# Performance work log

Measured on AMD Instinct MI355X. Metric: run time of the kernel, lower is better.

Reference implementation:

```python
import jax, jax.numpy as jnp
import numpy as np

B, C, H, W = 8, 512, 64, 64
RED = 4
CR = C // RED  # 128

def setup_inputs() -> dict:
    key = jax.random.key(0)
    k1, k2, k3 = jax.random.split(key, 3)
    x = jax.random.normal(k1, (B, C, H, W), dtype=jnp.float32)
    # conv_in: 1x1 conv, no bias -> weight [3*CR, C]
    w_in = jax.random.normal(k2, (3 * CR, C), dtype=jnp.float32) * 0.02
    # conv_out: 1x1 conv, no bias -> weight [C, CR]
    w_out = jax.random.normal(k3, (C, CR), dtype=jnp.float32) * 0.02
    return {"x": x, "w_in": w_in, "w_out": w_out}

def reference(x, w_in, w_out):
    b, c, h, w = x.shape
    n = h * w
    xf = x.reshape(b, c, n)                         # flatten spatial -> [B,C,N]
    proj = jnp.einsum('oc,bcn->bon', w_in, xf)      # 1x1 conv_in -> [B,3*CR,N]
    emb_a, emb_b, g = jnp.split(proj, 3, axis=1)    # each [B,CR,N]
    # unscaled full self-attention over N spatial tokens
    weights = jnp.einsum('bcn,bcm->bnm', emb_a, emb_b)   # [B,N,N]
    weights = jax.nn.softmax(weights, axis=2)
    y = jnp.einsum('bnm,bcm->bnc', weights, g)           # [B,N,CR]
    y = jnp.einsum('oc,bnc->bon', w_out, y)              # 1x1 conv_out -> [B,C,N]
    return x + y.reshape(b, c, h, w)
```

## Files before the change

kernel.cpp:

```cpp
#include <hip/hip_runtime.h>


typedef __attribute__((ext_vector_type(8))) short short8;
typedef __attribute__((ext_vector_type(4))) float f32x4;
typedef __attribute__((ext_vector_type(16))) float f32x16;
typedef __attribute__((ext_vector_type(2))) unsigned int uint2v;

__device__ inline unsigned bfr(float f) {
  union { float f; unsigned u; } v; v.f = f;
  return v.u + 0x8000u;
}
__device__ inline unsigned short f2bf(float f) { return (unsigned short)(bfr(f) >> 16); }
__device__ inline unsigned pack2(float a, float b) {
  return __builtin_amdgcn_perm(bfr(b), bfr(a), 0x07060302u);
}
__device__ inline unsigned cvtpk(float a, float b) {
  unsigned r;
  asm("v_cvt_pk_bf16_f32 %0, %1, %2" : "=v"(r) : "v"(a), "v"(b));
  return r;
}
__device__ inline int sw(int row, int col, int stride_halves) {
  return row * stride_halves + ((((col >> 3) ^ (row & 7)) << 3) | (col & 7));
}
__device__ inline void load_lds16(const void* g, void* l) {
  __builtin_amdgcn_global_load_lds(
      (const __attribute__((address_space(1))) unsigned int*)g,
      (__attribute__((address_space(3))) unsigned int*)l, 16, 0, 0);
}

__global__ __launch_bounds__(256) void k_prep(const float* __restrict__ w_in,
                                              const float* __restrict__ w_out,
                                              unsigned short* __restrict__ wi,
                                              unsigned short* __restrict__ wo) {
  int i = blockIdx.x * 256 + threadIdx.x;
  const float* src;
  unsigned short* dst;
  int base;
  float s = 1.0f;
  if (i < 24576) {
    src = w_in;  dst = wi; base = i * 8;
    if (base < 128 * 512) s = 1.4426950408889634f;
  } else {
    src = w_out; dst = wo; base = (i - 24576) * 8;
  }
  float4 d0 = *(const float4*)&src[base];
  float4 d1 = *(const float4*)&src[base + 4];
  d0.x *= s; d0.y *= s; d0.z *= s; d0.w *= s;
  d1.x *= s; d1.y *= s; d1.z *= s; d1.w *= s;
  uint4 p;
  p.x = pack2(d0.x, d0.y); p.y = pack2(d0.z, d0.w);
  p.z = pack2(d1.x, d1.y); p.w = pack2(d1.z, d1.w);
  *(uint4*)&dst[base] = p;
}

__global__ __launch_bounds__(256) void k_proj(const float* __restrict__ x,
                                              const unsigned short* __restrict__ wi,
                                              unsigned short* __restrict__ ab,
                                              unsigned short* __restrict__ gC) {
  __shared__ unsigned short A_lds[128 * 64];
  __shared__ unsigned short B_lds[64 * 64];
  const int t = threadIdx.x;
  const int lane = t & 63;
  const int w = t >> 6;
  const int l15 = lane & 15;
  const int quad = lane >> 4;
  const int n0 = blockIdx.x * 64;
  const int o0 = blockIdx.y * 128;
  const int b = blockIdx.z;
  const int ch8g = t >> 5;
  const int tp = t & 31;

  f32x4 acc[2][4];
#pragma unroll
  for (int i = 0; i < 2; i++)
#pragma unroll
    for (int j = 0; j < 4; j++) acc[i][j] = (f32x4)0.f;

  for (int k0 = 0; k0 < 512; k0 += 64) {
#pragma unroll
    for (int j = 0; j < 4; j++) {
      int row = w * 32 + j * 8 + (lane >> 3);
      int gs = (lane & 7) ^ (row & 7);
      load_lds16(&wi[(size_t)(o0 + row) * 512 + k0 + gs * 8],
                 (void*)&A_lds[(w * 32 + j * 8) * 64]);
    }
    {
      float2 d[8];
#pragma unroll
      for (int j = 0; j < 8; j++)
        d[j] = *(const float2*)&x[((size_t)(b * 512 + k0 + ch8g * 8 + j)) * 4096 + n0 + tp * 2];
#pragma unroll
      for (int i = 0; i < 2; i++) {
        int r = tp * 2 + i;
        uint4 pv;
        if (i == 0) {
          pv.x = pack2(d[0].x, d[1].x); pv.y = pack2(d[2].x, d[3].x);
          pv.z = pack2(d[4].x, d[5].x); pv.w = pack2(d[6].x, d[7].x);
        } else {
          pv.x = pack2(d[0].y, d[1].y); pv.y = pack2(d[2].y, d[3].y);
          pv.z = pack2(d[4].y, d[5].y); pv.w = pack2(d[6].y, d[7].y);
        }
        *(uint4*)&B_lds[sw(r, ch8g * 8, 64)] = pv;
      }
    }
    __syncthreads();
#pragma unroll
    for (int kk = 0; kk < 64; kk += 32) {
      short8 a0 = *(const short8*)&A_lds[sw(w * 32 + l15, kk + quad * 8, 64)];
      short8 a1 = *(const short8*)&A_lds[sw(w * 32 + 16 + l15, kk + quad * 8, 64)];
#pragma unroll
      for (int ns = 0; ns < 4; ns++) {
        short8 bb = *(const short8*)&B_lds[sw(ns * 16 + l15, kk + quad * 8, 64)];
        acc[0][ns] = __builtin_amdgcn_mfma_f32_16x16x32_bf16(a0, bb, acc[0][ns], 0, 0, 0);
        acc[1][ns] = __builtin_amdgcn_mfma_f32_16x16x32_bf16(a1, bb, acc[1][ns], 0, 0, 0);
      }
    }
    __syncthreads();
  }
  if (o0 < 256) {
#pragma unroll
    for (int ms = 0; ms < 2; ms++) {
      int o = o0 + w * 32 + ms * 16 + quad * 4;
#pragma unroll
      for (int ns = 0; ns < 4; ns++) {
        int n = n0 + ns * 16 + l15;
        uint2 p;
        p.x = pack2(acc[ms][ns][0], acc[ms][ns][1]);
        p.y = pack2(acc[ms][ns][2], acc[ms][ns][3]);
        *(uint2*)&ab[((size_t)(b * 4096 + n)) * 256 + o] = p;
      }
    }
  } else {
#pragma unroll
    for (int ms = 0; ms < 2; ms++) {
      int og = w * 32 + ms * 16 + quad * 4;
#pragma unroll
      for (int ns = 0; ns < 4; ns++) {
        int n = n0 + ns * 16 + l15;
#pragma unroll
        for (int r = 0; r < 4; r++)
          gC[((size_t)(b * 128 + og + r)) * 4096 + n] = f2bf(acc[ms][ns][r]);
      }
    }
  }
}

__global__ __launch_bounds__(256, 2) void k_attn(const unsigned short* __restrict__ ab,
                                                 const unsigned short* __restrict__ gC,
                                                 unsigned short* __restrict__ yt) {
  __shared__ uint4 smem4[65536 / 16];
  unsigned short* smem_h = (unsigned short*)smem4;
  float* Obuf = (float*)smem4;
  float* lsumbuf = (float*)((char*)smem4 + 33024);
  unsigned* Pbuf = (unsigned*)((char*)smem4 + 33280);

  const int t = threadIdx.x;
  const int lane = t & 63;
  const int w = t >> 6;
  const int wr = w & 1;
  const int wc = w >> 1;
  const int l31 = lane & 31;
  const int h = lane >> 5;
  const int l7 = l31 & 7;
  const int b = blockIdx.x & 7;
  const int q0 = (blockIdx.x >> 3) * 64;

  short8 qf[8];
  {
    const unsigned short* qp = &ab[((size_t)(b * 4096 + q0 + wc * 32 + l31)) * 256 + h * 8];
#pragma unroll
    for (int ks = 0; ks < 8; ks++) qf[ks] = *(const short8*)&qp[ks * 16];
  }

  const int krow_c = w * 16 + (lane >> 4);
  const int vrow_c = w * 32 + (lane >> 3);

  auto dma_tile = [&](int kt, int buf) {
    unsigned short* Kb = smem_h + buf * 8192;
    unsigned short* Vb = smem_h + 16384 + buf * 8192;
#pragma unroll
    for (int j = 0; j < 4; j++) {
      int row = krow_c + j * 4;
      int gs = (lane & 15) ^ (row & 7);
      load_lds16(&ab[((size_t)(b * 4096 + kt + row)) * 256 + 128 + gs * 8],
                 (void*)&Kb[(w * 16 + j * 4) * 128]);
    }
#pragma unroll
    for (int j = 0; j < 4; j++) {
      int row = vrow_c + j * 8;
      int gs = (lane & 7) ^ (row & 7);
      load_lds16(&gC[((size_t)(b * 128 + row)) * 4096 + kt + gs * 8],
                 (void*)&Vb[(w * 32 + j * 8) * 64]);
    }
  };

  f32x16 O[4];
#pragma unroll
  for (int i = 0; i < 4; i++) O[i] = (f32x16)0.f;
  float ls0 = 0.f, ls1 = 0.f, ls2 = 0.f, ls3 = 0.f;
  const int rowK = wr * 32 + l31;

  dma_tile(0, 0);
  __syncthreads();

  for (int it = 0; it < 64; ++it) {
    if (it < 63) dma_tile((it + 1) * 64, (it + 1) & 1);
    const unsigned short* Kc = smem_h + (it & 1) * 8192;
    const unsigned short* Vc = smem_h + 16384 + (it & 1) * 8192;

    f32x16 accS = (f32x16)0.f;
    __builtin_amdgcn_s_setprio(1);
#pragma unroll
    for (int ks = 0; ks < 8; ks++) {
      short8 ak = *(const short8*)&Kc[rowK * 128 + (((ks * 2 + h) ^ l7) << 3)];
      accS = __builtin_amdgcn_mfma_f32_32x32x16_bf16(ak, qf[ks], accS, 0, 0, 0);
    }
    __builtin_amdgcn_s_setprio(0);

    float ps[16];
#pragma unroll
    for (int r = 0; r < 16; r++) ps[r] = __builtin_amdgcn_exp2f(accS[r]);
    ls0 += ps[0] + ps[4];  ls1 += ps[1] + ps[5];
    ls2 += ps[2] + ps[6];  ls3 += ps[3] + ps[7];
    ls0 += ps[8] + ps[12]; ls1 += ps[9] + ps[13];
    ls2 += ps[10] + ps[14]; ls3 += ps[11] + ps[15];
    unsigned u[8];
#pragma unroll
    for (int i = 0; i < 8; i++) u[i] = cvtpk(ps[2 * i], ps[2 * i + 1]);

    short8 pfrag[2];
#pragma unroll
    for (int f = 0; f < 2; f++) {
      uint2v r02 = __builtin_amdgcn_permlane32_swap(u[4 * f + 0], u[4 * f + 2], false, false);
      uint2v r13 = __builtin_amdgcn_permlane32_swap(u[4 * f + 1], u[4 * f + 3], false, false);
      union { unsigned uu[4]; short8 s; } cv;
      cv.uu[0] = r02[0]; cv.uu[1] = r13[0]; cv.uu[2] = r02[1]; cv.uu[3] = r13[1];
      pfrag[f] = cv.s;
    }

    __builtin_amdgcn_s_setprio(1);
#pragma unroll
    for (int ct = 0; ct < 4; ct++) {
      int rowV = ct * 32 + l31;
#pragma unroll
      for (int f = 0; f < 2; f++) {
        short8 av = *(const short8*)&Vc[rowV * 64 + (((wr * 4 + f * 2 + h) ^ l7) << 3)];
        O[ct] = __builtin_amdgcn_mfma_f32_32x32x16_bf16(av, pfrag[f], O[ct], 0, 0, 0);
      }
    }
    __builtin_amdgcn_s_setprio(0);
    __syncthreads();
  }

  float lsum = (ls0 + ls1) + (ls2 + ls3);
  lsum += __shfl_xor(lsum, 32);
  const int q = wc * 32 + l31;
  if (wr == 0) {
#pragma unroll
    for (int ct = 0; ct < 4; ct++)
#pragma unroll
      for (int r = 0; r < 16; r++) {
        int c = ct * 32 + (r & 3) + 8 * (r >> 2) + 4 * h;
        Obuf[q * 129 + c] = O[ct][r];
      }
    if (h == 0) lsumbuf[q] = lsum;
  }
  __syncthreads();
  if (wr == 1) {
    float linv = 1.f / (lsum + lsumbuf[q]);
#pragma unroll
    for (int ct = 0; ct < 4; ct++)
#pragma unroll
      for (int r = 0; r < 16; r += 2) {
        int c = ct * 32 + (r & 3) + 8 * (r >> 2) + 4 * h;
        float v0 = (Obuf[q * 129 + c] + O[ct][r]) * linv;
        float v1 = (Obuf[q * 129 + c + 1] + O[ct][r + 1]) * linv;
        Pbuf[q * 65 + (c >> 1)] = pack2(v0, v1);
      }
  }
  __syncthreads();
  {
    int qq = t >> 2, seg = t & 3;
    unsigned* yrow = (unsigned*)&yt[((size_t)(b * 4096 + q0 + qq)) * 128];
#pragma unroll
    for (int i = 0; i < 4; i++) {
      uint4 v;
      v.x = Pbuf[qq * 65 + seg * 16 + i * 4 + 0];
      v.y = Pbuf[qq * 65 + seg * 16 + i * 4 + 1];
      v.z = Pbuf[qq * 65 + seg * 16 + i * 4 + 2];
      v.w = Pbuf[qq * 65 + seg * 16 + i * 4 + 3];
      *(uint4*)&yrow[seg * 16 + i * 4] = v;
    }
  }
}

__global__ __launch_bounds__(256) void k_out(const float* __restrict__ x,
                                             const unsigned short* __restrict__ wo,
                                             const unsigned short* __restrict__ yt,
                                             float* __restrict__ out) {
  __shared__ unsigned short A_lds[128 * 128];
  __shared__ unsigned short B_lds[64 * 128];
  const int t = threadIdx.x;
  const int lane = t & 63;
  const int w = t >> 6;
  const int l15 = lane & 15;
  const int quad = lane >> 4;
  const int n0 = blockIdx.x * 64;
  const int o0 = blockIdx.y * 128;
  const int b = blockIdx.z;

#pragma unroll
  for (int j = 0; j < 8; j++) {
    int row = w * 32 + j * 4 + (lane >> 4);
    int gs = (lane & 15) ^ (row & 7);
    load_lds16(&wo[(size_t)(o0 + row) * 128 + gs * 8],
               (void*)&A_lds[(w * 32 + j * 4) * 128]);
  }
#pragma unroll
  for (int j = 0; j < 4; j++) {
    int row = w * 16 + j * 4 + (lane >> 4);
    int gs = (lane & 15) ^ (row & 7);
    load_lds16(&yt[((size_t)(b * 4096 + n0 + row)) * 128 + gs * 8],
               (void*)&B_lds[(w * 16 + j * 4) * 128]);
  }
  __syncthreads();

  f32x4 acc[2][4];
#pragma unroll
  for (int i = 0; i < 2; i++)
#pragma unroll
    for (int j = 0; j < 4; j++) acc[i][j] = (f32x4)0.f;
#pragma unroll
  for (int ks = 0; ks < 4; ks++) {
    short8 a0 = *(const short8*)&A_lds[sw(w * 32 + l15, ks * 32 + quad * 8, 128)];
    short8 a1 = *(const short8*)&A_lds[sw(w * 32 + 16 + l15, ks * 32 + quad * 8, 128)];
#pragma unroll
    for (int ns = 0; ns < 4; ns++) {
      short8 bb = *(const short8*)&B_lds[sw(ns * 16 + l15, ks * 32 + quad * 8, 128)];
      acc[0][ns] = __builtin_amdgcn_mfma_f32_16x16x32_bf16(a0, bb, acc[0][ns], 0, 0, 0);
      acc[1][ns] = __builtin_amdgcn_mfma_f32_16x16x32_bf16(a1, bb, acc[1][ns], 0, 0, 0);
    }
  }
#pragma unroll
  for (int ms = 0; ms < 2; ms++) {
    int o = o0 + w * 32 + ms * 16 + quad * 4;
#pragma unroll
    for (int ns = 0; ns < 4; ns++) {
      int n = n0 + ns * 16 + l15;
#pragma unroll
      for (int r = 0; r < 4; r++) {
        size_t off = ((size_t)(b * 512 + o + r)) * 4096 + n;
        out[off] = x[off] + acc[ms][ns][r];
      }
    }
  }
}

extern "C" void kernel_launch(void* const* d_in, const int* in_sizes, int n_in,
                              void* d_out, int out_size, void* d_ws, size_t ws_size,
                              hipStream_t stream) {
  const float* x = (const float*)d_in[0];
  const float* w_in = (const float*)d_in[1];
  const float* w_out = (const float*)d_in[2];
  float* out = (float*)d_out;

  unsigned short* ab = (unsigned short*)d_ws;
  unsigned short* gC = ab + (size_t)8 * 4096 * 256;
  unsigned short* yt = gC + (size_t)8 * 128 * 4096;
  unsigned short* wi = yt + (size_t)8 * 4096 * 128;
  unsigned short* wo = wi + (size_t)384 * 512;

  k_prep<<<128, 256, 0, stream>>>(w_in, w_out, wi, wo);
  k_proj<<<dim3(64, 3, 8), 256, 0, stream>>>(x, wi, ab, gC);
  k_attn<<<dim3(512), 256, 0, stream>>>(ab, gC, yt);
  k_out<<<dim3(64, 4, 8), 256, 0, stream>>>(x, wo, yt, out);
}
```

Measured before the change: 233.3 us.

## Process two query sub-tiles per attention block to reuse K/V tiles

Each attention block now handles 128 queries instead of 64, holding two sets of Q fragments and output accumulators per wave. Every K and V tile loaded into LDS is reused for two MFMA chains, which halves global K/V traffic and the number of LDS tile loads per query. In exchange register pressure doubles, so launch bounds drop to one block per SIMD group, the grid halves to 256 blocks (fewer than two per CU on 256 CUs), and the epilogue runs twice with extra barriers.

```diff
diff --git a/kernel.cpp b/kernel.cpp
--- a/kernel.cpp
+++ b/kernel.cpp
@@ -145,7 +145,7 @@
   }
 }
 
-__global__ __launch_bounds__(256, 2) void k_attn(const unsigned short* __restrict__ ab,
+__global__ __launch_bounds__(256, 1) void k_attn(const unsigned short* __restrict__ ab,
                                                  const unsigned short* __restrict__ gC,
                                                  unsigned short* __restrict__ yt) {
   __shared__ uint4 smem4[65536 / 16];
@@ -163,13 +163,15 @@
   const int h = lane >> 5;
   const int l7 = l31 & 7;
   const int b = blockIdx.x & 7;
-  const int q0 = (blockIdx.x >> 3) * 64;
-
-  short8 qf[8];
-  {
-    const unsigned short* qp = &ab[((size_t)(b * 4096 + q0 + wc * 32 + l31)) * 256 + h * 8];
-#pragma unroll
-    for (int ks = 0; ks < 8; ks++) qf[ks] = *(const short8*)&qp[ks * 16];
+  const int q0 = (blockIdx.x >> 3) * 128;
+
+  short8 qf[2][8];
+#pragma unroll
+  for (int sub = 0; sub < 2; sub++) {
+    const unsigned short* qp =
+        &ab[((size_t)(b * 4096 + q0 + wc * 64 + sub * 32 + l31)) * 256 + h * 8];
+#pragma unroll
+    for (int ks = 0; ks < 8; ks++) qf[sub][ks] = *(const short8*)&qp[ks * 16];
   }
 
   const int krow_c = w * 16 + (lane >> 4);
@@ -194,10 +196,12 @@
     }
   };
 
-  f32x16 O[4];
-#pragma unroll
-  for (int i = 0; i < 4; i++) O[i] = (f32x16)0.f;
-  float ls0 = 0.f, ls1 = 0.f, ls2 = 0.f, ls3 = 0.f;
+  f32x16 O[2][4];
+#pragma unroll
+  for (int s = 0; s < 2; s++)
+#pragma unroll
+    for (int i = 0; i < 4; i++) O[s][i] = (f32x16)0.f;
+  float lsA[2] = {0.f, 0.f}, lsB[2] = {0.f, 0.f};
   const int rowK = wr * 32 + l31;
 
   dma_tile(0, 0);
@@ -208,34 +212,36 @@
     const unsigned short* Kc = smem_h + (it & 1) * 8192;
     const unsigned short* Vc = smem_h + 16384 + (it & 1) * 8192;
 
-    f32x16 accS = (f32x16)0.f;
+    f32x16 accS0 = (f32x16)0.f, accS1 = (f32x16)0.f;
     __builtin_amdgcn_s_setprio(1);
 #pragma unroll
     for (int ks = 0; ks < 8; ks++) {
       short8 ak = *(const short8*)&Kc[rowK * 128 + (((ks * 2 + h) ^ l7) << 3)];
-      accS = __builtin_amdgcn_mfma_f32_32x32x16_bf16(ak, qf[ks], accS, 0, 0, 0);
+      accS0 = __builtin_amdgcn_mfma_f32_32x32x16_bf16(ak, qf[0][ks], accS0, 0, 0, 0);
+      accS1 = __builtin_amdgcn_mfma_f32_32x32x16_bf16(ak, qf[1][ks], accS1, 0, 0, 0);
     }
     __builtin_amdgcn_s_setprio(0);
 
-    float ps[16];
-#pragma unroll
-    for (int r = 0; r < 16; r++) ps[r] = __builtin_amdgcn_exp2f(accS[r]);
-    ls0 += ps[0] + ps[4];  ls1 += ps[1] + ps[5];
-    ls2 += ps[2] + ps[6];  ls3 += ps[3] + ps[7];
-    ls0 += ps[8] + ps[12]; ls1 += ps[9] + ps[13];
-    ls2 += ps[10] + ps[14]; ls3 += ps[11] + ps[15];
-    unsigned u[8];
-#pragma unroll
-    for (int i = 0; i < 8; i++) u[i] = cvtpk(ps[2 * i], ps[2 * i + 1]);
-
-    short8 pfrag[2];
-#pragma unroll
-    for (int f = 0; f < 2; f++) {
-      uint2v r02 = __builtin_amdgcn_permlane32_swap(u[4 * f + 0], u[4 * f + 2], false, false);
-      uint2v r13 = __builtin_amdgcn_permlane32_swap(u[4 * f + 1], u[4 * f + 3], false, false);
-      union { unsigned uu[4]; short8 s; } cv;
-      cv.uu[0] = r02[0]; cv.uu[1] = r13[0]; cv.uu[2] = r02[1]; cv.uu[3] = r13[1];
-      pfrag[f] = cv.s;
+    short8 pf[2][2];
+#pragma unroll
+    for (int sub = 0; sub < 2; sub++) {
+      const f32x16 aS = sub ? accS1 : accS0;
+      float ps[16];
+#pragma unroll
+      for (int r = 0; r < 16; r++) ps[r] = __builtin_amdgcn_exp2f(aS[r]);
+      lsA[sub] += ((ps[0] + ps[4]) + (ps[8] + ps[12])) + ((ps[2] + ps[6]) + (ps[10] + ps[14]));
+      lsB[sub] += ((ps[1] + ps[5]) + (ps[9] + ps[13])) + ((ps[3] + ps[7]) + (ps[11] + ps[15]));
+      unsigned u[8];
+#pragma unroll
+      for (int i = 0; i < 8; i++) u[i] = cvtpk(ps[2 * i], ps[2 * i + 1]);
+#pragma unroll
+      for (int f = 0; f < 2; f++) {
+        uint2v r02 = __builtin_amdgcn_permlane32_swap(u[4 * f + 0], u[4 * f + 2], false, false);
+        uint2v r13 = __builtin_amdgcn_permlane32_swap(u[4 * f + 1], u[4 * f + 3], false, false);
+        union { unsigned uu[4]; short8 s; } cv;
+        cv.uu[0] = r02[0]; cv.uu[1] = r13[0]; cv.uu[2] = r02[1]; cv.uu[3] = r13[1];
+        pf[sub][f] = cv.s;
+      }
     }
 
     __builtin_amdgcn_s_setprio(1);
@@ -245,52 +251,58 @@
 #pragma unroll
       for (int f = 0; f < 2; f++) {
         short8 av = *(const short8*)&Vc[rowV * 64 + (((wr * 4 + f * 2 + h) ^ l7) << 3)];
-        O[ct] = __builtin_amdgcn_mfma_f32_32x32x16_bf16(av, pfrag[f], O[ct], 0, 0, 0);
+        O[0][ct] = __builtin_amdgcn_mfma_f32_32x32x16_bf16(av, pf[0][f], O[0][ct], 0, 0, 0);
+        O[1][ct] = __builtin_amdgcn_mfma_f32_32x32x16_bf16(av, pf[1][f], O[1][ct], 0, 0, 0);
       }
     }
     __builtin_amdgcn_s_setprio(0);
     __syncthreads();
   }
 
-  float lsum = (ls0 + ls1) + (ls2 + ls3);
-  lsum += __shfl_xor(lsum, 32);
-  const int q = wc * 32 + l31;
-  if (wr == 0) {
-#pragma unroll
-    for (int ct = 0; ct < 4; ct++)
-#pragma unroll
-      for (int r = 0; r < 16; r++) {
-        int c = ct * 32 + (r & 3) + 8 * (r >> 2) + 4 * h;
-        Obuf[q * 129 + c] = O[ct][r];
-      }
-    if (h == 0) lsumbuf[q] = lsum;
-  }
-  __syncthreads();
-  if (wr == 1) {
-    float linv = 1.f / (lsum + lsumbuf[q]);
-#pragma unroll
-    for (int ct = 0; ct < 4; ct++)
-#pragma unroll
-      for (int r = 0; r < 16; r += 2) {
-        int c = ct * 32 + (r & 3) + 8 * (r >> 2) + 4 * h;
-        float v0 = (Obuf[q * 129 + c] + O[ct][r]) * linv;
-        float v1 = (Obuf[q * 129 + c + 1] + O[ct][r + 1]) * linv;
-        Pbuf[q * 65 + (c >> 1)] = pack2(v0, v1);
-      }
-  }
-  __syncthreads();
-  {
-    int qq = t >> 2, seg = t & 3;
-    unsigned* yrow = (unsigned*)&yt[((size_t)(b * 4096 + q0 + qq)) * 128];
-#pragma unroll
-    for (int i = 0; i < 4; i++) {
-      uint4 v;
-      v.x = Pbuf[qq * 65 + seg * 16 + i * 4 + 0];
-      v.y = Pbuf[qq * 65 + seg * 16 + i * 4 + 1];
-      v.z = Pbuf[qq * 65 + seg * 16 + i * 4 + 2];
-      v.w = Pbuf[qq * 65 + seg * 16 + i * 4 + 3];
-      *(uint4*)&yrow[seg * 16 + i * 4] = v;
-    }
+#pragma unroll
+  for (int sub = 0; sub < 2; sub++) {
+    float lsum = lsA[sub] + lsB[sub];
+    lsum += __shfl_xor(lsum, 32);
+    const int qb = wc * 32 + l31;
+    if (wr == 0) {
+#pragma unroll
+      for (int ct = 0; ct < 4; ct++)
+#pragma unroll
+        for (int r = 0; r < 16; r++) {
+          int c = ct * 32 + (r & 3) + 8 * (r >> 2) + 4 * h;
+          Obuf[qb * 129 + c] = O[sub][ct][r];
+        }
+      if (h == 0) lsumbuf[qb] = lsum;
+    }
+    __syncthreads();
+    if (wr == 1) {
+      float linv = 1.f / (lsum + lsumbuf[qb]);
+#pragma unroll
+      for (int ct = 0; ct < 4; ct++)
+#pragma unroll
+        for (int r = 0; r < 16; r += 2) {
+          int c = ct * 32 + (r & 3) + 8 * (r >> 2) + 4 * h;
+          float v0 = (Obuf[qb * 129 + c] + O[sub][ct][r]) * linv;
+          float v1 = (Obuf[qb * 129 + c + 1] + O[sub][ct][r + 1]) * linv;
+          Pbuf[qb * 65 + (c >> 1)] = pack2(v0, v1);
+        }
+    }
+    __syncthreads();
+    {
+      int qq = t >> 2, seg = t & 3;
+      int qreal = q0 + ((qq >> 5) << 6) + sub * 32 + (qq & 31);
+      unsigned* yrow = (unsigned*)&yt[((size_t)(b * 4096 + qreal)) * 128];
+#pragma unroll
+      for (int i = 0; i < 4; i++) {
+        uint4 v;
+        v.x = Pbuf[qq * 65 + seg * 16 + i * 4 + 0];
+        v.y = Pbuf[qq * 65 + seg * 16 + i * 4 + 1];
+        v.z = Pbuf[qq * 65 + seg * 16 + i * 4 + 2];
+        v.w = Pbuf[qq * 65 + seg * 16 + i * 4 + 3];
+        *(uint4*)&yrow[seg * 16 + i * 4] = v;
+      }
+    }
+    if (sub == 0) __syncthreads();
   }
 }
 
@@ -372,6 +384,6 @@
 
   k_prep<<<128, 256, 0, stream>>>(w_in, w_out, wi, wo);
   k_proj<<<dim3(64, 3, 8), 256, 0, stream>>>(x, wi, ab, gC);
-  k_attn<<<dim3(512), 256, 0, stream>>>(ab, gC, yt);
+  k_attn<<<dim3(256), 256, 0, stream>>>(ab, gC, yt);
   k_out<<<dim3(64, 4, 8), 256, 0, stream>>>(x, wo, yt, out);
 }
```

Result: slower. 250.5 us (+7.4%).

## Load V fragments directly from global into registers and prefetch x in projection

Applied to the files above, without the earlier changes.

The attention kernel no longer stages V tiles through LDS. Each wave loads its V fragments straight from global memory into registers every iteration, which frees 16 KB of shared memory and removes the LDS reads for V. In the projection GEMM, the x tile for the next k-step is loaded into registers ahead of time, so global latency overlaps with compute. The cost is direct global loads of V on the critical path with no double buffering, plus higher register pressure.

```diff
diff --git a/kernel.cpp b/kernel.cpp
--- a/kernel.cpp
+++ b/kernel.cpp
@@ -76,6 +76,11 @@
 #pragma unroll
     for (int j = 0; j < 4; j++) acc[i][j] = (f32x4)0.f;
 
+  float2 d[8];
+#pragma unroll
+  for (int j = 0; j < 8; j++)
+    d[j] = *(const float2*)&x[((size_t)(b * 512 + ch8g * 8 + j)) * 4096 + n0 + tp * 2];
+
   for (int k0 = 0; k0 < 512; k0 += 64) {
 #pragma unroll
     for (int j = 0; j < 4; j++) {
@@ -84,24 +89,23 @@
       load_lds16(&wi[(size_t)(o0 + row) * 512 + k0 + gs * 8],
                  (void*)&A_lds[(w * 32 + j * 8) * 64]);
     }
-    {
-      float2 d[8];
+#pragma unroll
+    for (int i = 0; i < 2; i++) {
+      int r = tp * 2 + i;
+      uint4 pv;
+      if (i == 0) {
+        pv.x = pack2(d[0].x, d[1].x); pv.y = pack2(d[2].x, d[3].x);
+        pv.z = pack2(d[4].x, d[5].x); pv.w = pack2(d[6].x, d[7].x);
+      } else {
+        pv.x = pack2(d[0].y, d[1].y); pv.y = pack2(d[2].y, d[3].y);
+        pv.z = pack2(d[4].y, d[5].y); pv.w = pack2(d[6].y, d[7].y);
+      }
+      *(uint4*)&B_lds[sw(r, ch8g * 8, 64)] = pv;
+    }
+    if (k0 + 64 < 512) {
 #pragma unroll
       for (int j = 0; j < 8; j++)
-        d[j] = *(const float2*)&x[((size_t)(b * 512 + k0 + ch8g * 8 + j)) * 4096 + n0 + tp * 2];
-#pragma unroll
-      for (int i = 0; i < 2; i++) {
-        int r = tp * 2 + i;
-        uint4 pv;
-        if (i == 0) {
-          pv.x = pack2(d[0].x, d[1].x); pv.y = pack2(d[2].x, d[3].x);
-          pv.z = pack2(d[4].x, d[5].x); pv.w = pack2(d[6].x, d[7].x);
-        } else {
-          pv.x = pack2(d[0].y, d[1].y); pv.y = pack2(d[2].y, d[3].y);
-          pv.z = pack2(d[4].y, d[5].y); pv.w = pack2(d[6].y, d[7].y);
-        }
-        *(uint4*)&B_lds[sw(r, ch8g * 8, 64)] = pv;
-      }
+        d[j] = *(const float2*)&x[((size_t)(b * 512 + k0 + 64 + ch8g * 8 + j)) * 4096 + n0 + tp * 2];
     }
     __syncthreads();
 #pragma unroll
@@ -148,7 +152,7 @@
 __global__ __launch_bounds__(256, 2) void k_attn(const unsigned short* __restrict__ ab,
                                                  const unsigned short* __restrict__ gC,
                                                  unsigned short* __restrict__ yt) {
-  __shared__ uint4 smem4[65536 / 16];
+  __shared__ uint4 smem4[50176 / 16];
   unsigned short* smem_h = (unsigned short*)smem4;
   float* Obuf = (float*)smem4;
   float* lsumbuf = (float*)((char*)smem4 + 33024);
@@ -173,11 +177,8 @@
   }
 
   const int krow_c = w * 16 + (lane >> 4);
-  const int vrow_c = w * 32 + (lane >> 3);
-
-  auto dma_tile = [&](int kt, int buf) {
+  auto dma_k = [&](int kt, int buf) {
     unsigned short* Kb = smem_h + buf * 8192;
-    unsigned short* Vb = smem_h + 16384 + buf * 8192;
 #pragma unroll
     for (int j = 0; j < 4; j++) {
       int row = krow_c + j * 4;
@@ -185,13 +186,6 @@
       load_lds16(&ab[((size_t)(b * 4096 + kt + row)) * 256 + 128 + gs * 8],
                  (void*)&Kb[(w * 16 + j * 4) * 128]);
     }
-#pragma unroll
-    for (int j = 0; j < 4; j++) {
-      int row = vrow_c + j * 8;
-      int gs = (lane & 7) ^ (row & 7);
-      load_lds16(&gC[((size_t)(b * 128 + row)) * 4096 + kt + gs * 8],
-                 (void*)&Vb[(w * 32 + j * 8) * 64]);
-    }
   };
 
   f32x16 O[4];
@@ -199,14 +193,24 @@
   for (int i = 0; i < 4; i++) O[i] = (f32x16)0.f;
   float ls0 = 0.f, ls1 = 0.f, ls2 = 0.f, ls3 = 0.f;
   const int rowK = wr * 32 + l31;
-
-  dma_tile(0, 0);
+  const int vG = wr * 4 + h;
+  const unsigned short* vrow0 = &gC[((size_t)(b * 128 + l31)) * 4096];
+
+  dma_k(0, 0);
   __syncthreads();
 
   for (int it = 0; it < 64; ++it) {
-    if (it < 63) dma_tile((it + 1) * 64, (it + 1) & 1);
+    const int kt = it * 64;
+    if (it < 63) dma_k(kt + 64, (it + 1) & 1);
+
+    short8 vreg[4][2];
+#pragma unroll
+    for (int ct = 0; ct < 4; ct++)
+#pragma unroll
+      for (int f = 0; f < 2; f++)
+        vreg[ct][f] = *(const short8*)&vrow0[(size_t)ct * 32 * 4096 + kt + (vG + f * 2) * 8];
+
     const unsigned short* Kc = smem_h + (it & 1) * 8192;
-    const unsigned short* Vc = smem_h + 16384 + (it & 1) * 8192;
 
     f32x16 accS = (f32x16)0.f;
     __builtin_amdgcn_s_setprio(1);
@@ -241,11 +245,9 @@
     __builtin_amdgcn_s_setprio(1);
 #pragma unroll
     for (int ct = 0; ct < 4; ct++) {
-      int rowV = ct * 32 + l31;
 #pragma unroll
       for (int f = 0; f < 2; f++) {
-        short8 av = *(const short8*)&Vc[rowV * 64 + (((wr * 4 + f * 2 + h) ^ l7) << 3)];
-        O[ct] = __builtin_amdgcn_mfma_f32_32x32x16_bf16(av, pfrag[f], O[ct], 0, 0, 0);
+        O[ct] = __builtin_amdgcn_mfma_f32_32x32x16_bf16(vreg[ct][f], pfrag[f], O[ct], 0, 0, 0);
       }
     }
     __builtin_amdgcn_s_setprio(0);
```

Result: slower. 291.9 us (+25.1%).

## Compute all 384 projection channels per block to reuse x tile, prefetch x

Applied to the files above, without the earlier changes.

The projection kernel now computes all three outputs (a, b, g, 384 channels) per block instead of splitting them across a grid dimension. Each x tile is therefore read from global memory and converted to bf16 once rather than three times. The next x slice is register-prefetched while the current one is consumed. In exchange the grid shrinks to 512 blocks, each with a larger LDS weight tile (48KB), more accumulator registers, and a launch bound of 2, which may reduce occupancy.

```diff
diff --git a/kernel.cpp b/kernel.cpp
--- a/kernel.cpp
+++ b/kernel.cpp
@@ -53,11 +53,11 @@
   *(uint4*)&dst[base] = p;
 }
 
-__global__ __launch_bounds__(256) void k_proj(const float* __restrict__ x,
-                                              const unsigned short* __restrict__ wi,
-                                              unsigned short* __restrict__ ab,
-                                              unsigned short* __restrict__ gC) {
-  __shared__ unsigned short A_lds[128 * 64];
+__global__ __launch_bounds__(256, 2) void k_proj(const float* __restrict__ x,
+                                                 const unsigned short* __restrict__ wi,
+                                                 unsigned short* __restrict__ ab,
+                                                 unsigned short* __restrict__ gC) {
+  __shared__ unsigned short A_lds[384 * 64];
   __shared__ unsigned short B_lds[64 * 64];
   const int t = threadIdx.x;
   const int lane = t & 63;
@@ -65,81 +65,84 @@
   const int l15 = lane & 15;
   const int quad = lane >> 4;
   const int n0 = blockIdx.x * 64;
-  const int o0 = blockIdx.y * 128;
-  const int b = blockIdx.z;
+  const int b = blockIdx.y;
   const int ch8g = t >> 5;
   const int tp = t & 31;
 
-  f32x4 acc[2][4];
-#pragma unroll
-  for (int i = 0; i < 2; i++)
+  f32x4 acc[6][4];
+#pragma unroll
+  for (int i = 0; i < 6; i++)
 #pragma unroll
     for (int j = 0; j < 4; j++) acc[i][j] = (f32x4)0.f;
 
+  float2 d[8];
+#pragma unroll
+  for (int j = 0; j < 8; j++)
+    d[j] = *(const float2*)&x[((size_t)(b * 512 + ch8g * 8 + j)) * 4096 + n0 + tp * 2];
+
   for (int k0 = 0; k0 < 512; k0 += 64) {
 #pragma unroll
-    for (int j = 0; j < 4; j++) {
-      int row = w * 32 + j * 8 + (lane >> 3);
+    for (int j = 0; j < 12; j++) {
+      int row = w * 96 + j * 8 + (lane >> 3);
       int gs = (lane & 7) ^ (row & 7);
-      load_lds16(&wi[(size_t)(o0 + row) * 512 + k0 + gs * 8],
-                 (void*)&A_lds[(w * 32 + j * 8) * 64]);
-    }
-    {
-      float2 d[8];
+      load_lds16(&wi[(size_t)row * 512 + k0 + gs * 8],
+                 (void*)&A_lds[(w * 96 + j * 8) * 64]);
+    }
+#pragma unroll
+    for (int i = 0; i < 2; i++) {
+      int r = tp * 2 + i;
+      uint4 pv;
+      if (i == 0) {
+        pv.x = pack2(d[0].x, d[1].x); pv.y = pack2(d[2].x, d[3].x);
+        pv.z = pack2(d[4].x, d[5].x); pv.w = pack2(d[6].x, d[7].x);
+      } else {
+        pv.x = pack2(d[0].y, d[1].y); pv.y = pack2(d[2].y, d[3].y);
+        pv.z = pack2(d[4].y, d[5].y); pv.w = pack2(d[6].y, d[7].y);
+      }
+      *(uint4*)&B_lds[sw(r, ch8g * 8, 64)] = pv;
+    }
+    if (k0 + 64 < 512) {
 #pragma unroll
       for (int j = 0; j < 8; j++)
-        d[j] = *(const float2*)&x[((size_t)(b * 512 + k0 + ch8g * 8 + j)) * 4096 + n0 + tp * 2];
-#pragma unroll
-      for (int i = 0; i < 2; i++) {
-        int r = tp * 2 + i;
-        uint4 pv;
-        if (i == 0) {
-          pv.x = pack2(d[0].x, d[1].x); pv.y = pack2(d[2].x, d[3].x);
-          pv.z = pack2(d[4].x, d[5].x); pv.w = pack2(d[6].x, d[7].x);
-        } else {
-          pv.x = pack2(d[0].y, d[1].y); pv.y = pack2(d[2].y, d[3].y);
-          pv.z = pack2(d[4].y, d[5].y); pv.w = pack2(d[6].y, d[7].y);
-        }
-        *(uint4*)&B_lds[sw(r, ch8g * 8, 64)] = pv;
-      }
+        d[j] = *(const float2*)&x[((size_t)(b * 512 + k0 + 64 + ch8g * 8 + j)) * 4096 + n0 + tp * 2];
     }
     __syncthreads();
 #pragma unroll
     for (int kk = 0; kk < 64; kk += 32) {
-      short8 a0 = *(const short8*)&A_lds[sw(w * 32 + l15, kk + quad * 8, 64)];
-      short8 a1 = *(const short8*)&A_lds[sw(w * 32 + 16 + l15, kk + quad * 8, 64)];
+      short8 a[6];
+#pragma unroll
+      for (int m = 0; m < 6; m++)
+        a[m] = *(const short8*)&A_lds[sw(w * 96 + m * 16 + l15, kk + quad * 8, 64)];
 #pragma unroll
       for (int ns = 0; ns < 4; ns++) {
         short8 bb = *(const short8*)&B_lds[sw(ns * 16 + l15, kk + quad * 8, 64)];
-        acc[0][ns] = __builtin_amdgcn_mfma_f32_16x16x32_bf16(a0, bb, acc[0][ns], 0, 0, 0);
-        acc[1][ns] = __builtin_amdgcn_mfma_f32_16x16x32_bf16(a1, bb, acc[1][ns], 0, 0, 0);
+#pragma unroll
+        for (int m = 0; m < 6; m++)
+          acc[m][ns] = __builtin_amdgcn_mfma_f32_16x16x32_bf16(a[m], bb, acc[m][ns], 0, 0, 0);
       }
     }
     __syncthreads();
   }
-  if (o0 < 256) {
-#pragma unroll
-    for (int ms = 0; ms < 2; ms++) {
-      int o = o0 + w * 32 + ms * 16 + quad * 4;
+#pragma unroll
+  for (int m = 0; m < 6; m++) {
+    int o = w * 96 + m * 16 + quad * 4;
+    if (o < 256) {
 #pragma unroll
       for (int ns = 0; ns < 4; ns++) {
         int n = n0 + ns * 16 + l15;
         uint2 p;
-        p.x = pack2(acc[ms][ns][0], acc[ms][ns][1]);
-        p.y = pack2(acc[ms][ns][2], acc[ms][ns][3]);
+        p.x = pack2(acc[m][ns][0], acc[m][ns][1]);
+        p.y = pack2(acc[m][ns][2], acc[m][ns][3]);
         *(uint2*)&ab[((size_t)(b * 4096 + n)) * 256 + o] = p;
       }
-    }
-  } else {
-#pragma unroll
-    for (int ms = 0; ms < 2; ms++) {
-      int og = w * 32 + ms * 16 + quad * 4;
+    } else {
+      int og = o - 256;
 #pragma unroll
       for (int ns = 0; ns < 4; ns++) {
         int n = n0 + ns * 16 + l15;
 #pragma unroll
         for (int r = 0; r < 4; r++)
-          gC[((size_t)(b * 128 + og + r)) * 4096 + n] = f2bf(acc[ms][ns][r]);
+          gC[((size_t)(b * 128 + og + r)) * 4096 + n] = f2bf(acc[m][ns][r]);
       }
     }
   }
@@ -371,7 +374,7 @@
   unsigned short* wo = wi + (size_t)384 * 512;
 
   k_prep<<<128, 256, 0, stream>>>(w_in, w_out, wi, wo);
-  k_proj<<<dim3(64, 3, 8), 256, 0, stream>>>(x, wi, ab, gC);
+  k_proj<<<dim3(64, 8), 256, 0, stream>>>(x, wi, ab, gC);
   k_attn<<<dim3(512), 256, 0, stream>>>(ab, gC, yt);
   k_out<<<dim3(64, 4, 8), 256, 0, stream>>>(x, wo, yt, out);
 }
```

Result: faster. 227.7 us (-2.4%).
